# Kernel tuning notes

Measured on AMD Instinct MI355X. Metric: run time of the kernel, lower is better.

Reference implementation:

```python
import jax, jax.numpy as jnp
import numpy as np

HIDDEN = 1024
HEADS = 16
HEAD_DIM = HIDDEN // HEADS
LN_EPS = 1e-5


def setup_inputs() -> dict:
    key = jax.random.key(0)
    ks = jax.random.split(key, 8)
    B, S = 4, 2048
    s = 1.0 / np.sqrt(HIDDEN)
    return {
        "x": jax.random.normal(ks[0], (B, S, HIDDEN), dtype=jnp.float32),
        "Wq": jax.random.normal(ks[1], (HIDDEN, HIDDEN), dtype=jnp.float32) * s,
        "bq": jax.random.normal(ks[2], (HIDDEN,), dtype=jnp.float32) * 0.01,
        "Wk": jax.random.normal(ks[3], (HIDDEN, HIDDEN), dtype=jnp.float32) * s,
        "bk": jax.random.normal(ks[4], (HIDDEN,), dtype=jnp.float32) * 0.01,
        "Wv": jax.random.normal(ks[5], (HIDDEN, HIDDEN), dtype=jnp.float32) * s,
        "bv": jax.random.normal(ks[6], (HIDDEN,), dtype=jnp.float32) * 0.01,
        "gamma": jnp.ones((HIDDEN,), dtype=jnp.float32),
        "beta": jnp.zeros((HIDDEN,), dtype=jnp.float32),
    }


def reference(x, Wq, bq, Wk, bk, Wv, bv, gamma, beta):
    B, S, H = x.shape
    # LayerNorm
    mu = jnp.mean(x, axis=-1, keepdims=True)
    var = jnp.mean(jnp.square(x - mu), axis=-1, keepdims=True)
    xn = (x - mu) / jnp.sqrt(var + LN_EPS) * gamma + beta
    # QKV projections -> [B, heads, S, head_dim]
    def split_heads(t):
        return t.reshape(B, S, HEADS, HEAD_DIM).transpose(0, 2, 1, 3)
    q = split_heads(xn @ Wq + bq)
    k = split_heads(xn @ Wk + bk)
    v = split_heads(xn @ Wv + bv)
    scores = jnp.einsum("bhqd,bhkd->bhqk", q, k) / np.sqrt(HEAD_DIM)
    probs = jax.nn.softmax(scores, axis=-1)
    attended = jnp.einsum("bhqk,bhkd->bhqd", probs, v)
    attended = attended.transpose(0, 2, 1, 3).reshape(B, S, H)
    # residual (dropout = 0.0 / eval mode is identity)
    return xn + attended
```

## Files before the change

kernel.cpp:

```cpp
#include <hip/hip_runtime.h>
#include <hip/hip_bf16.h>

#define HIDDEN 1024
#define HEADS 16
#define HEAD_DIM 64
#define SEQ 2048
#define BATCH 4

typedef __attribute__((ext_vector_type(8))) short bf16x8;
typedef __attribute__((ext_vector_type(4))) float f32x4;
typedef __attribute__((ext_vector_type(16))) float f32x16;
typedef __attribute__((ext_vector_type(4))) short short4v;

static __device__ __forceinline__ unsigned short f2bf(float f) {
  union { float f; unsigned u; } u;
  u.f = f;
  unsigned r = u.u + 0x7fffu + ((u.u >> 16) & 1u);
  return (unsigned short)(r >> 16);
}

static __device__ __forceinline__ float bf2f(short s) {
  union { unsigned u; float f; } t;
  t.u = ((unsigned)(unsigned short)s) << 16;
  return t.f;
}

static __device__ __forceinline__ unsigned packtr(float lo, float hi) {
  union { float f; unsigned u; } a, b;
  a.f = lo; b.f = hi;
#if __has_builtin(__builtin_amdgcn_perm)
  return __builtin_amdgcn_perm(b.u, a.u, 0x07060302u);
#else
  return (b.u & 0xFFFF0000u) | (a.u >> 16);
#endif
}

static __device__ __forceinline__ bf16x8 frag4(unsigned u0, unsigned u1,
                                               unsigned u2, unsigned u3) {
  union { unsigned u[4]; bf16x8 v; } t;
  t.u[0] = u0; t.u[1] = u1; t.u[2] = u2; t.u[3] = u3;
  return t.v;
}

static __device__ __forceinline__ float fexp2(float x) {
#if __has_builtin(__builtin_amdgcn_exp2f)
  return __builtin_amdgcn_exp2f(x);
#else
  return exp2f(x);
#endif
}

typedef const __attribute__((address_space(1))) unsigned int* gp1_t;
typedef __attribute__((address_space(3))) unsigned int* lp3_t;
static __device__ __forceinline__ void gload_lds16(const void* g, void* l) {
  __builtin_amdgcn_global_load_lds((gp1_t)g, (lp3_t)l, 16, 0, 0);
}

__global__ __launch_bounds__(256) void prep_kernel(
    const float* __restrict__ x, const float* __restrict__ gamma,
    const float* __restrict__ beta, unsigned short* __restrict__ xnb,
    const float* __restrict__ Wq, const float* __restrict__ Wk,
    const float* __restrict__ Wv, unsigned short* __restrict__ Wt) {
  __shared__ float tile[64][65];
  int bid = blockIdx.x;
  int tid = threadIdx.x;
  if (bid < BATCH * SEQ) {
    int row = bid;
    const float4* xr = (const float4*)(x + (size_t)row * HIDDEN);
    float4 v = xr[tid];
    float s = v.x + v.y + v.z + v.w;
    float sq = v.x * v.x + v.y * v.y + v.z * v.z + v.w * v.w;
#pragma unroll
    for (int off = 32; off >= 1; off >>= 1) {
      s += __shfl_xor(s, off);
      sq += __shfl_xor(sq, off);
    }
    int wave = tid >> 6, lane = tid & 63;
    if (lane == 0) { tile[0][wave] = s; tile[0][4 + wave] = sq; }
    __syncthreads();
    s = tile[0][0] + tile[0][1] + tile[0][2] + tile[0][3];
    sq = tile[0][4] + tile[0][5] + tile[0][6] + tile[0][7];
    float mu = s * (1.0f / HIDDEN);
    float var = sq * (1.0f / HIDDEN) - mu * mu;
    float rstd = rsqrtf(var + 1e-5f);
    float4 g = ((const float4*)gamma)[tid];
    float4 bt = ((const float4*)beta)[tid];
    short4v p;
    p.x = (short)f2bf((v.x - mu) * rstd * g.x + bt.x);
    p.y = (short)f2bf((v.y - mu) * rstd * g.y + bt.y);
    p.z = (short)f2bf((v.z - mu) * rstd * g.z + bt.z);
    p.w = (short)f2bf((v.w - mu) * rstd * g.w + bt.w);
    *((short4v*)(xnb + (size_t)row * HIDDEN) + tid) = p;
  } else {
    int w = bid - BATCH * SEQ;
    int z = w >> 8, rem = w & 255;
    int k0 = (rem & 15) * 64, n0 = (rem >> 4) * 64;
    const float* W = (z == 0) ? Wq : (z == 1) ? Wk : Wv;
    int tr = tid >> 4;
    int tc = tid & 15;
#pragma unroll
    for (int p = 0; p < 4; ++p) {
      int kk = p * 16 + tr;
      float4 v = *(const float4*)(W + (size_t)(k0 + kk) * HIDDEN + n0 + tc * 4);
      tile[kk][tc * 4 + 0] = v.x; tile[kk][tc * 4 + 1] = v.y;
      tile[kk][tc * 4 + 2] = v.z; tile[kk][tc * 4 + 3] = v.w;
    }
    __syncthreads();
    unsigned short* op = Wt + (size_t)z * HIDDEN * HIDDEN;
#pragma unroll
    for (int p = 0; p < 4; ++p) {
      int nn = p * 16 + tr;
      short4v o;
      o.x = (short)f2bf(tile[tc * 4 + 0][nn]);
      o.y = (short)f2bf(tile[tc * 4 + 1][nn]);
      o.z = (short)f2bf(tile[tc * 4 + 2][nn]);
      o.w = (short)f2bf(tile[tc * 4 + 3][nn]);
      *(short4v*)(op + (size_t)(n0 + nn) * HIDDEN + k0 + tc * 4) = o;
    }
  }
}

__global__ __launch_bounds__(512) void qkv_gemm(
    const unsigned short* __restrict__ xnb, const unsigned short* __restrict__ Wt,
    const float* __restrict__ bq, const float* __restrict__ bk,
    const float* __restrict__ bv, unsigned short* __restrict__ qO,
    unsigned short* __restrict__ kO, unsigned short* __restrict__ vtO) {
  __shared__ unsigned short As[2][128 * 64];
  __shared__ unsigned short Bs[2][128 * 64];
  int z = blockIdx.z;
  int m0 = blockIdx.x * 128;
  int n0 = blockIdx.y * 128;
  int tid = threadIdx.x;
  int wave = tid >> 6, lane = tid & 63;
  int lr = lane & 15, g = lane >> 4;
  int wm = wave >> 2, wn = wave & 3;
  const unsigned short* Ab = xnb + (size_t)m0 * HIDDEN;
  const unsigned short* Bb = Wt + (size_t)z * HIDDEN * HIDDEN + (size_t)n0 * HIDDEN;
  int srow = wave * 8 + (lane >> 3);
  int scol = ((lane & 7) ^ (lane >> 3)) << 3;
  f32x4 acc[4][2];
#pragma unroll
  for (int i = 0; i < 4; ++i)
#pragma unroll
    for (int j = 0; j < 2; ++j) acc[i][j] = (f32x4){0.f, 0.f, 0.f, 0.f};

#pragma unroll
  for (int i = 0; i < 2; ++i) {
    int row = i * 64 + srow;
    gload_lds16(Ab + (size_t)row * HIDDEN + scol, &As[0][row * 64]);
    gload_lds16(Bb + (size_t)row * HIDDEN + scol, &Bs[0][row * 64]);
  }
  __syncthreads();

#pragma unroll 1
  for (int t = 0; t < 16; ++t) {
    int cur = t & 1;
    if (t < 15) {
      int k1 = (t + 1) * 64;
#pragma unroll
      for (int i = 0; i < 2; ++i) {
        int row = i * 64 + srow;
        gload_lds16(Ab + (size_t)row * HIDDEN + k1 + scol, &As[cur ^ 1][row * 64]);
        gload_lds16(Bb + (size_t)row * HIDDEN + k1 + scol, &Bs[cur ^ 1][row * 64]);
      }
    }
    bf16x8 aF[4][2], bF[2][2];
#pragma unroll
    for (int mb = 0; mb < 4; ++mb) {
      int row = wm * 64 + mb * 16 + lr;
#pragma unroll
      for (int ks = 0; ks < 2; ++ks)
        aF[mb][ks] = *(const bf16x8*)&As[cur][row * 64 + (((ks * 4 + g) ^ (row & 7)) << 3)];
    }
#pragma unroll
    for (int nb = 0; nb < 2; ++nb) {
      int row = wn * 32 + nb * 16 + lr;
#pragma unroll
      for (int ks = 0; ks < 2; ++ks)
        bF[nb][ks] = *(const bf16x8*)&Bs[cur][row * 64 + (((ks * 4 + g) ^ (row & 7)) << 3)];
    }
#pragma unroll
    for (int ks = 0; ks < 2; ++ks)
#pragma unroll
      for (int mb = 0; mb < 4; ++mb)
#pragma unroll
        for (int nb = 0; nb < 2; ++nb)
          acc[mb][nb] = __builtin_amdgcn_mfma_f32_16x16x32_bf16(aF[mb][ks], bF[nb][ks], acc[mb][nb], 0, 0, 0);
    __syncthreads();
  }
  const float* bias = (z == 0) ? bq : (z == 1) ? bk : bv;
  if (z == 2) {
#pragma unroll
    for (int nb = 0; nb < 2; ++nb) {
      int n = n0 + wn * 32 + nb * 16 + lr;
      float bsv = bias[n];
      int h = n >> 6, d = n & 63;
#pragma unroll
      for (int mb = 0; mb < 4; ++mb) {
        int m = m0 + wm * 64 + mb * 16 + g * 4;
        int bb = m >> 11, sIdx = m & 2047;
        short4v pk;
        pk.x = (short)f2bf(acc[mb][nb][0] + bsv);
        pk.y = (short)f2bf(acc[mb][nb][1] + bsv);
        pk.z = (short)f2bf(acc[mb][nb][2] + bsv);
        pk.w = (short)f2bf(acc[mb][nb][3] + bsv);
        *(short4v*)(vtO + (size_t)((bb * HEADS + h) * HEAD_DIM + d) * SEQ + sIdx) = pk;
      }
    }
  } else {
    unsigned short* outp = (z == 0) ? qO : kO;
    float scale = (z == 0) ? 0.18033688011112042f : 1.0f;
#pragma unroll
    for (int nb = 0; nb < 2; ++nb) {
      int n = n0 + wn * 32 + nb * 16 + lr;
      float bsv = bias[n];
      int h = n >> 6, d = n & 63;
#pragma unroll
      for (int mb = 0; mb < 4; ++mb) {
#pragma unroll
        for (int r = 0; r < 4; ++r) {
          int m = m0 + wm * 64 + mb * 16 + g * 4 + r;
          int bb = m >> 11, sIdx = m & 2047;
          unsigned short bits = f2bf((acc[mb][nb][r] + bsv) * scale);
          outp[(size_t)((bb * HEADS + h) * SEQ + sIdx) * HEAD_DIM + d] = bits;
        }
      }
    }
  }
}

static __device__ __forceinline__ void attn_subtile(
    const unsigned short* __restrict__ Kb, const unsigned short* __restrict__ Vb,
    const int (&koff)[4], const bf16x8 (&qF)[4],
    const f32x16& ZERO, f32x16& o0, f32x16& o1, float& lsum) {
  f32x16 sc0, sc1;
  __builtin_amdgcn_s_setprio(1);
  {
    bf16x8 k0 = *(const bf16x8*)&Kb[koff[0]];
    bf16x8 k1 = *(const bf16x8*)&Kb[koff[0] + 2048];
    sc0 = __builtin_amdgcn_mfma_f32_32x32x16_bf16(k0, qF[0], ZERO, 0, 0, 0);
    sc1 = __builtin_amdgcn_mfma_f32_32x32x16_bf16(k1, qF[0], ZERO, 0, 0, 0);
  }
#pragma unroll
  for (int s = 1; s < 4; ++s) {
    bf16x8 k0 = *(const bf16x8*)&Kb[koff[s]];
    bf16x8 k1 = *(const bf16x8*)&Kb[koff[s] + 2048];
    sc0 = __builtin_amdgcn_mfma_f32_32x32x16_bf16(k0, qF[s], sc0, 0, 0, 0);
    sc1 = __builtin_amdgcn_mfma_f32_32x32x16_bf16(k1, qF[s], sc1, 0, 0, 0);
  }
  __builtin_amdgcn_s_setprio(0);
#pragma unroll
  for (int s = 0; s < 4; ++s) {
    float e[8];
#pragma unroll
    for (int j = 0; j < 8; ++j) {
      float scv = (s < 2) ? sc0[8 * s + j] : sc1[8 * (s - 2) + j];
      e[j] = fexp2(scv);
    }
    lsum += ((e[0] + e[1]) + (e[2] + e[3])) + ((e[4] + e[5]) + (e[6] + e[7]));
    unsigned pa0 = packtr(e[0], e[1]);
    unsigned pb0 = packtr(e[2], e[3]);
    unsigned pa1 = packtr(e[4], e[5]);
    unsigned pb1 = packtr(e[6], e[7]);
#if __has_builtin(__builtin_amdgcn_permlane32_swap)
    auto ra = __builtin_amdgcn_permlane32_swap(pa0, pa1, false, false);
    auto rb = __builtin_amdgcn_permlane32_swap(pb0, pb1, false, false);
    bf16x8 pF = frag4(ra[0], rb[0], ra[1], rb[1]);
#else
    int hf = (threadIdx.x & 63) >> 5;
    unsigned t0 = __shfl_xor(hf ? pa0 : pa1, 32);
    unsigned t1 = __shfl_xor(hf ? pb0 : pb1, 32);
    bf16x8 pF = frag4(hf ? t0 : pa0, hf ? t1 : pb0,
                      hf ? pa1 : t0, hf ? pb1 : t1);
#endif
    bf16x8 v0 = *(const bf16x8*)&Vb[koff[s]];
    bf16x8 v1 = *(const bf16x8*)&Vb[koff[s] + 2048];
    __builtin_amdgcn_s_setprio(1);
    o0 = __builtin_amdgcn_mfma_f32_32x32x16_bf16(v0, pF, o0, 0, 0, 0);
    o1 = __builtin_amdgcn_mfma_f32_32x32x16_bf16(v1, pF, o1, 0, 0, 0);
    __builtin_amdgcn_s_setprio(0);
  }
}

__global__ __launch_bounds__(512, 4) void attn_kernel(
    const unsigned short* __restrict__ qB, const unsigned short* __restrict__ kB,
    const unsigned short* __restrict__ vtB, const unsigned short* __restrict__ xnb,
    float* __restrict__ out) {
  __shared__ unsigned short Kt[2][2][64 * 64];
  __shared__ unsigned short Vt[2][2][64 * 64];
  int orig = blockIdx.y * gridDim.x + blockIdx.x;
  int swz = (orig & 7) * 64 + (orig >> 3);
  int bx = swz & 7;
  int by = swz >> 3;
  int b = by >> 4, hh = by & 15;
  int tid = threadIdx.x, wave = tid >> 6, lane = tid & 63;
  int lq = lane & 31;
  int hf = lane >> 5;
  int q0 = bx * 256 + wave * 32;
  const unsigned short* qh = qB + (size_t)by * SEQ * HEAD_DIM;
  const unsigned short* kh = kB + (size_t)by * SEQ * HEAD_DIM;
  const unsigned short* vh = vtB + (size_t)by * HEAD_DIM * SEQ;

  bf16x8 qF[4];
#pragma unroll
  for (int s = 0; s < 4; ++s)
    qF[s] = *(const bf16x8*)(qh + (size_t)(q0 + lq) * HEAD_DIM + s * 16 + hf * 8);

  int srow = wave * 8 + (lane >> 3);
  int scoff = ((lane & 7) ^ (lane >> 3)) << 3;
  int xorb = (lq & 7) << 4;
  int koff[4];
#pragma unroll
  for (int s = 0; s < 4; ++s)
    koff[s] = (lq * 128 + ((s * 32 + hf * 16) ^ xorb)) >> 1;

  f32x16 o0, o1, ZERO;
#pragma unroll
  for (int r = 0; r < 16; ++r) { o0[r] = 0.f; o1[r] = 0.f; ZERO[r] = 0.f; }
  float lsum = 0.f;

#pragma unroll
  for (int sub = 0; sub < 2; ++sub) {
    gload_lds16(kh + (size_t)(sub * 64 + srow) * HEAD_DIM + scoff, &Kt[0][sub][wave * 512]);
    gload_lds16(vh + (size_t)srow * SEQ + sub * 64 + scoff, &Vt[0][sub][wave * 512]);
  }
  __syncthreads();

#pragma unroll 1
  for (int t = 0; t < 16; ++t) {
    int cur = t & 1;
    if (t < 15) {
      int kv1 = (t + 1) * 128;
#pragma unroll
      for (int sub = 0; sub < 2; ++sub) {
        gload_lds16(kh + (size_t)(kv1 + sub * 64 + srow) * HEAD_DIM + scoff,
                    &Kt[cur ^ 1][sub][wave * 512]);
        gload_lds16(vh + (size_t)srow * SEQ + kv1 + sub * 64 + scoff,
                    &Vt[cur ^ 1][sub][wave * 512]);
      }
    }
    attn_subtile(Kt[cur][0], Vt[cur][0], koff, qF, ZERO, o0, o1, lsum);
    attn_subtile(Kt[cur][1], Vt[cur][1], koff, qF, ZERO, o0, o1, lsum);
    __syncthreads();
  }
  lsum += __shfl_xor(lsum, 32);
  float inv = 1.0f / lsum;
  size_t rowbase = ((size_t)b * SEQ + q0 + lq) * HIDDEN + hh * HEAD_DIM;
  const unsigned short* xrow = xnb + rowbase;
  float* orow = out + rowbase;
#pragma unroll
  for (int qd = 0; qd < 4; ++qd) {
    int d0 = qd * 8 + 4 * hf;
    short4v xa = *(const short4v*)(xrow + d0);
    short4v xb = *(const short4v*)(xrow + 32 + d0);
    float4 oa, ob;
    oa.x = bf2f(xa.x) + o0[qd * 4 + 0] * inv;
    oa.y = bf2f(xa.y) + o0[qd * 4 + 1] * inv;
    oa.z = bf2f(xa.z) + o0[qd * 4 + 2] * inv;
    oa.w = bf2f(xa.w) + o0[qd * 4 + 3] * inv;
    ob.x = bf2f(xb.x) + o1[qd * 4 + 0] * inv;
    ob.y = bf2f(xb.y) + o1[qd * 4 + 1] * inv;
    ob.z = bf2f(xb.z) + o1[qd * 4 + 2] * inv;
    ob.w = bf2f(xb.w) + o1[qd * 4 + 3] * inv;
    *(float4*)(orow + d0) = oa;
    *(float4*)(orow + 32 + d0) = ob;
  }
}

extern "C" void kernel_launch(void* const* d_in, const int* in_sizes, int n_in,
                              void* d_out, int out_size, void* d_ws, size_t ws_size,
                              hipStream_t stream) {
  const float* x     = (const float*)d_in[0];
  const float* Wq    = (const float*)d_in[1];
  const float* bq    = (const float*)d_in[2];
  const float* Wk    = (const float*)d_in[3];
  const float* bk    = (const float*)d_in[4];
  const float* Wv    = (const float*)d_in[5];
  const float* bv    = (const float*)d_in[6];
  const float* gamma = (const float*)d_in[7];
  const float* beta  = (const float*)d_in[8];
  float* out = (float*)d_out;
  char* ws = (char*)d_ws;
  const size_t MB = 1024 * 1024;
  unsigned short* xnb = (unsigned short*)(ws);
  unsigned short* Wt  = (unsigned short*)(ws + 16 * MB);
  unsigned short* qb  = (unsigned short*)(ws + 22 * MB);
  unsigned short* kb  = (unsigned short*)(ws + 38 * MB);
  unsigned short* vtb = (unsigned short*)(ws + 54 * MB);

  hipLaunchKernelGGL(prep_kernel, dim3(BATCH * SEQ + 768), dim3(256), 0, stream,
                     x, gamma, beta, xnb, Wq, Wk, Wv, Wt);
  hipLaunchKernelGGL(qkv_gemm, dim3(64, 8, 3), dim3(512), 0, stream, xnb, Wt, bq, bk, bv, qb, kb, vtb);
  hipLaunchKernelGGL(attn_kernel, dim3(8, 64), dim3(512), 0, stream, qb, kb, vtb, xnb, out);
}
```

Baseline: 155.6 us.

## Process two 32-row query tiles per wave to reuse K/V fragments

Each wave now handles 64 query rows as two 32-row subtiles that share every K and V fragment read from LDS, so the block covers 512 queries and the grid is halved. This halves LDS reads and global K/V staging per query and gives more independent MFMAs to interleave. In exchange it doubles accumulator and score register use, lowers the occupancy hint from 4 to 2 blocks, and leaves only 256 blocks, which may underfill the GPU.

```diff
diff --git a/kernel.cpp b/kernel.cpp
--- a/kernel.cpp
+++ b/kernel.cpp
@@ -229,82 +229,105 @@
   }
 }
 
-static __device__ __forceinline__ void attn_subtile(
+static __device__ __forceinline__ void attn_subtile2(
     const unsigned short* __restrict__ Kb, const unsigned short* __restrict__ Vb,
-    const int (&koff)[4], const bf16x8 (&qF)[4],
-    const f32x16& ZERO, f32x16& o0, f32x16& o1, float& lsum) {
-  f32x16 sc0, sc1;
+    const int (&koff)[4], const bf16x8 (&qFA)[4], const bf16x8 (&qFB)[4],
+    const f32x16& ZERO, f32x16& o0A, f32x16& o1A, f32x16& o0B, f32x16& o1B,
+    float& lsumA, float& lsumB) {
+  f32x16 sA0, sA1, sB0, sB1;
   __builtin_amdgcn_s_setprio(1);
   {
     bf16x8 k0 = *(const bf16x8*)&Kb[koff[0]];
     bf16x8 k1 = *(const bf16x8*)&Kb[koff[0] + 2048];
-    sc0 = __builtin_amdgcn_mfma_f32_32x32x16_bf16(k0, qF[0], ZERO, 0, 0, 0);
-    sc1 = __builtin_amdgcn_mfma_f32_32x32x16_bf16(k1, qF[0], ZERO, 0, 0, 0);
+    sA0 = __builtin_amdgcn_mfma_f32_32x32x16_bf16(k0, qFA[0], ZERO, 0, 0, 0);
+    sA1 = __builtin_amdgcn_mfma_f32_32x32x16_bf16(k1, qFA[0], ZERO, 0, 0, 0);
+    sB0 = __builtin_amdgcn_mfma_f32_32x32x16_bf16(k0, qFB[0], ZERO, 0, 0, 0);
+    sB1 = __builtin_amdgcn_mfma_f32_32x32x16_bf16(k1, qFB[0], ZERO, 0, 0, 0);
   }
 #pragma unroll
   for (int s = 1; s < 4; ++s) {
     bf16x8 k0 = *(const bf16x8*)&Kb[koff[s]];
     bf16x8 k1 = *(const bf16x8*)&Kb[koff[s] + 2048];
-    sc0 = __builtin_amdgcn_mfma_f32_32x32x16_bf16(k0, qF[s], sc0, 0, 0, 0);
-    sc1 = __builtin_amdgcn_mfma_f32_32x32x16_bf16(k1, qF[s], sc1, 0, 0, 0);
+    sA0 = __builtin_amdgcn_mfma_f32_32x32x16_bf16(k0, qFA[s], sA0, 0, 0, 0);
+    sA1 = __builtin_amdgcn_mfma_f32_32x32x16_bf16(k1, qFA[s], sA1, 0, 0, 0);
+    sB0 = __builtin_amdgcn_mfma_f32_32x32x16_bf16(k0, qFB[s], sB0, 0, 0, 0);
+    sB1 = __builtin_amdgcn_mfma_f32_32x32x16_bf16(k1, qFB[s], sB1, 0, 0, 0);
   }
   __builtin_amdgcn_s_setprio(0);
 #pragma unroll
   for (int s = 0; s < 4; ++s) {
-    float e[8];
+    float eA[8], eB[8];
 #pragma unroll
     for (int j = 0; j < 8; ++j) {
-      float scv = (s < 2) ? sc0[8 * s + j] : sc1[8 * (s - 2) + j];
-      e[j] = fexp2(scv);
-    }
-    lsum += ((e[0] + e[1]) + (e[2] + e[3])) + ((e[4] + e[5]) + (e[6] + e[7]));
-    unsigned pa0 = packtr(e[0], e[1]);
-    unsigned pb0 = packtr(e[2], e[3]);
-    unsigned pa1 = packtr(e[4], e[5]);
-    unsigned pb1 = packtr(e[6], e[7]);
+      float svA = (s < 2) ? sA0[8 * s + j] : sA1[8 * (s - 2) + j];
+      float svB = (s < 2) ? sB0[8 * s + j] : sB1[8 * (s - 2) + j];
+      eA[j] = fexp2(svA);
+      eB[j] = fexp2(svB);
+    }
+    lsumA += ((eA[0] + eA[1]) + (eA[2] + eA[3])) + ((eA[4] + eA[5]) + (eA[6] + eA[7]));
+    lsumB += ((eB[0] + eB[1]) + (eB[2] + eB[3])) + ((eB[4] + eB[5]) + (eB[6] + eB[7]));
+    unsigned a0 = packtr(eA[0], eA[1]);
+    unsigned a1 = packtr(eA[2], eA[3]);
+    unsigned a2 = packtr(eA[4], eA[5]);
+    unsigned a3 = packtr(eA[6], eA[7]);
+    unsigned b0 = packtr(eB[0], eB[1]);
+    unsigned b1 = packtr(eB[2], eB[3]);
+    unsigned b2 = packtr(eB[4], eB[5]);
+    unsigned b3 = packtr(eB[6], eB[7]);
 #if __has_builtin(__builtin_amdgcn_permlane32_swap)
-    auto ra = __builtin_amdgcn_permlane32_swap(pa0, pa1, false, false);
-    auto rb = __builtin_amdgcn_permlane32_swap(pb0, pb1, false, false);
-    bf16x8 pF = frag4(ra[0], rb[0], ra[1], rb[1]);
+    auto rAa = __builtin_amdgcn_permlane32_swap(a0, a2, false, false);
+    auto rAb = __builtin_amdgcn_permlane32_swap(a1, a3, false, false);
+    bf16x8 pFA = frag4(rAa[0], rAb[0], rAa[1], rAb[1]);
+    auto rBa = __builtin_amdgcn_permlane32_swap(b0, b2, false, false);
+    auto rBb = __builtin_amdgcn_permlane32_swap(b1, b3, false, false);
+    bf16x8 pFB = frag4(rBa[0], rBb[0], rBa[1], rBb[1]);
 #else
     int hf = (threadIdx.x & 63) >> 5;
-    unsigned t0 = __shfl_xor(hf ? pa0 : pa1, 32);
-    unsigned t1 = __shfl_xor(hf ? pb0 : pb1, 32);
-    bf16x8 pF = frag4(hf ? t0 : pa0, hf ? t1 : pb0,
-                      hf ? pa1 : t0, hf ? pb1 : t1);
+    unsigned tA0 = __shfl_xor(hf ? a0 : a2, 32);
+    unsigned tA1 = __shfl_xor(hf ? a1 : a3, 32);
+    bf16x8 pFA = frag4(hf ? tA0 : a0, hf ? tA1 : a1,
+                       hf ? a2 : tA0, hf ? a3 : tA1);
+    unsigned tB0 = __shfl_xor(hf ? b0 : b2, 32);
+    unsigned tB1 = __shfl_xor(hf ? b1 : b3, 32);
+    bf16x8 pFB = frag4(hf ? tB0 : b0, hf ? tB1 : b1,
+                       hf ? b2 : tB0, hf ? b3 : tB1);
 #endif
     bf16x8 v0 = *(const bf16x8*)&Vb[koff[s]];
     bf16x8 v1 = *(const bf16x8*)&Vb[koff[s] + 2048];
     __builtin_amdgcn_s_setprio(1);
-    o0 = __builtin_amdgcn_mfma_f32_32x32x16_bf16(v0, pF, o0, 0, 0, 0);
-    o1 = __builtin_amdgcn_mfma_f32_32x32x16_bf16(v1, pF, o1, 0, 0, 0);
+    o0A = __builtin_amdgcn_mfma_f32_32x32x16_bf16(v0, pFA, o0A, 0, 0, 0);
+    o1A = __builtin_amdgcn_mfma_f32_32x32x16_bf16(v1, pFA, o1A, 0, 0, 0);
+    o0B = __builtin_amdgcn_mfma_f32_32x32x16_bf16(v0, pFB, o0B, 0, 0, 0);
+    o1B = __builtin_amdgcn_mfma_f32_32x32x16_bf16(v1, pFB, o1B, 0, 0, 0);
     __builtin_amdgcn_s_setprio(0);
   }
 }
 
-__global__ __launch_bounds__(512, 4) void attn_kernel(
+__global__ __launch_bounds__(512, 2) void attn_kernel(
     const unsigned short* __restrict__ qB, const unsigned short* __restrict__ kB,
     const unsigned short* __restrict__ vtB, const unsigned short* __restrict__ xnb,
     float* __restrict__ out) {
   __shared__ unsigned short Kt[2][2][64 * 64];
   __shared__ unsigned short Vt[2][2][64 * 64];
   int orig = blockIdx.y * gridDim.x + blockIdx.x;
-  int swz = (orig & 7) * 64 + (orig >> 3);
-  int bx = swz & 7;
-  int by = swz >> 3;
+  int swz = (orig & 7) * 32 + (orig >> 3);
+  int bx = swz & 3;
+  int by = swz >> 2;
   int b = by >> 4, hh = by & 15;
   int tid = threadIdx.x, wave = tid >> 6, lane = tid & 63;
   int lq = lane & 31;
   int hf = lane >> 5;
-  int q0 = bx * 256 + wave * 32;
+  int q0 = bx * 512 + wave * 64;
   const unsigned short* qh = qB + (size_t)by * SEQ * HEAD_DIM;
   const unsigned short* kh = kB + (size_t)by * SEQ * HEAD_DIM;
   const unsigned short* vh = vtB + (size_t)by * HEAD_DIM * SEQ;
 
-  bf16x8 qF[4];
-#pragma unroll
-  for (int s = 0; s < 4; ++s)
-    qF[s] = *(const bf16x8*)(qh + (size_t)(q0 + lq) * HEAD_DIM + s * 16 + hf * 8);
+  bf16x8 qFA[4], qFB[4];
+#pragma unroll
+  for (int s = 0; s < 4; ++s) {
+    qFA[s] = *(const bf16x8*)(qh + (size_t)(q0 + lq) * HEAD_DIM + s * 16 + hf * 8);
+    qFB[s] = *(const bf16x8*)(qh + (size_t)(q0 + 32 + lq) * HEAD_DIM + s * 16 + hf * 8);
+  }
 
   int srow = wave * 8 + (lane >> 3);
   int scoff = ((lane & 7) ^ (lane >> 3)) << 3;
@@ -314,10 +337,12 @@
   for (int s = 0; s < 4; ++s)
     koff[s] = (lq * 128 + ((s * 32 + hf * 16) ^ xorb)) >> 1;
 
-  f32x16 o0, o1, ZERO;
-#pragma unroll
-  for (int r = 0; r < 16; ++r) { o0[r] = 0.f; o1[r] = 0.f; ZERO[r] = 0.f; }
-  float lsum = 0.f;
+  f32x16 o0A, o1A, o0B, o1B, ZERO;
+#pragma unroll
+  for (int r = 0; r < 16; ++r) {
+    o0A[r] = 0.f; o1A[r] = 0.f; o0B[r] = 0.f; o1B[r] = 0.f; ZERO[r] = 0.f;
+  }
+  float lsumA = 0.f, lsumB = 0.f;
 
 #pragma unroll
   for (int sub = 0; sub < 2; ++sub) {
@@ -339,31 +364,41 @@
                     &Vt[cur ^ 1][sub][wave * 512]);
       }
     }
-    attn_subtile(Kt[cur][0], Vt[cur][0], koff, qF, ZERO, o0, o1, lsum);
-    attn_subtile(Kt[cur][1], Vt[cur][1], koff, qF, ZERO, o0, o1, lsum);
+    attn_subtile2(Kt[cur][0], Vt[cur][0], koff, qFA, qFB, ZERO,
+                  o0A, o1A, o0B, o1B, lsumA, lsumB);
+    attn_subtile2(Kt[cur][1], Vt[cur][1], koff, qFA, qFB, ZERO,
+                  o0A, o1A, o0B, o1B, lsumA, lsumB);
     __syncthreads();
   }
-  lsum += __shfl_xor(lsum, 32);
-  float inv = 1.0f / lsum;
-  size_t rowbase = ((size_t)b * SEQ + q0 + lq) * HIDDEN + hh * HEAD_DIM;
-  const unsigned short* xrow = xnb + rowbase;
-  float* orow = out + rowbase;
-#pragma unroll
-  for (int qd = 0; qd < 4; ++qd) {
-    int d0 = qd * 8 + 4 * hf;
-    short4v xa = *(const short4v*)(xrow + d0);
-    short4v xb = *(const short4v*)(xrow + 32 + d0);
-    float4 oa, ob;
-    oa.x = bf2f(xa.x) + o0[qd * 4 + 0] * inv;
-    oa.y = bf2f(xa.y) + o0[qd * 4 + 1] * inv;
-    oa.z = bf2f(xa.z) + o0[qd * 4 + 2] * inv;
-    oa.w = bf2f(xa.w) + o0[qd * 4 + 3] * inv;
-    ob.x = bf2f(xb.x) + o1[qd * 4 + 0] * inv;
-    ob.y = bf2f(xb.y) + o1[qd * 4 + 1] * inv;
-    ob.z = bf2f(xb.z) + o1[qd * 4 + 2] * inv;
-    ob.w = bf2f(xb.w) + o1[qd * 4 + 3] * inv;
-    *(float4*)(orow + d0) = oa;
-    *(float4*)(orow + 32 + d0) = ob;
+  lsumA += __shfl_xor(lsumA, 32);
+  lsumB += __shfl_xor(lsumB, 32);
+  float invA = 1.0f / lsumA;
+  float invB = 1.0f / lsumB;
+#pragma unroll
+  for (int st = 0; st < 2; ++st) {
+    float inv = st ? invB : invA;
+    const f32x16& p0 = st ? o0B : o0A;
+    const f32x16& p1 = st ? o1B : o1A;
+    size_t rowbase = ((size_t)b * SEQ + q0 + st * 32 + lq) * HIDDEN + hh * HEAD_DIM;
+    const unsigned short* xrow = xnb + rowbase;
+    float* orow = out + rowbase;
+#pragma unroll
+    for (int qd = 0; qd < 4; ++qd) {
+      int d0 = qd * 8 + 4 * hf;
+      short4v xa = *(const short4v*)(xrow + d0);
+      short4v xb = *(const short4v*)(xrow + 32 + d0);
+      float4 oa, ob;
+      oa.x = bf2f(xa.x) + p0[qd * 4 + 0] * inv;
+      oa.y = bf2f(xa.y) + p0[qd * 4 + 1] * inv;
+      oa.z = bf2f(xa.z) + p0[qd * 4 + 2] * inv;
+      oa.w = bf2f(xa.w) + p0[qd * 4 + 3] * inv;
+      ob.x = bf2f(xb.x) + p1[qd * 4 + 0] * inv;
+      ob.y = bf2f(xb.y) + p1[qd * 4 + 1] * inv;
+      ob.z = bf2f(xb.z) + p1[qd * 4 + 2] * inv;
+      ob.w = bf2f(xb.w) + p1[qd * 4 + 3] * inv;
+      *(float4*)(orow + d0) = oa;
+      *(float4*)(orow + 32 + d0) = ob;
+    }
   }
 }
 
@@ -391,5 +426,5 @@
   hipLaunchKernelGGL(prep_kernel, dim3(BATCH * SEQ + 768), dim3(256), 0, stream,
                      x, gamma, beta, xnb, Wq, Wk, Wv, Wt);
   hipLaunchKernelGGL(qkv_gemm, dim3(64, 8, 3), dim3(512), 0, stream, xnb, Wt, bq, bk, bv, qb, kb, vtb);
-  hipLaunchKernelGGL(attn_kernel, dim3(8, 64), dim3(512), 0, stream, qb, kb, vtb, xnb, out);
-}
+  hipLaunchKernelGGL(attn_kernel, dim3(4, 64), dim3(512), 0, stream, qb, kb, vtb, xnb, out);
+}
```

Result: no change. 154.4 us (-0.8%).
